# Kernel tuning notes

Hardware: AMD Instinct MI355X
Metric: run time of the kernel (lower is better)

Reference implementation:

```python
import jax, jax.numpy as jnp
import numpy as np
from jax import lax

N, IC, OC, K, SDIM, H, W = 16, 512, 512, 3, 512, 32, 32
PAD, STRIDE, LR = 1, 1, 1.0
WEIGHT_SCALER = 1.0 / np.sqrt(IC * K * K) * LR   # equalized-lr conv scale
FC_SCALER = 1.0 / np.sqrt(SDIM) * LR             # equalized-lr fc scale


def setup_inputs() -> dict:
    key = jax.random.key(0)
    k1, k2, k3 = jax.random.split(key, 3)
    x = jax.random.normal(k1, (N, IC, H, W), dtype=jnp.float32)
    style = jax.random.normal(k2, (N, SDIM), dtype=jnp.float32)
    weight = jax.random.normal(k3, (OC, IC, K, K), dtype=jnp.float32)  # std = 1/lr = 1
    fc_weight = jax.random.normal(jax.random.fold_in(key, 10), (IC, SDIM), dtype=jnp.float32)
    fc_bias = jnp.zeros((IC,), dtype=jnp.float32)
    return {"x": x, "style": style, "weight": weight,
            "fc_weight": fc_weight, "fc_bias": fc_bias}


def reference(x, style, weight, fc_weight, fc_bias):
    # EqualizedFullyConnect + AddChannelwiseBias, then +1 -> modulation rates [N, iC]
    mod = jnp.einsum('ns,cs->nc', style, fc_weight) * FC_SCALER + fc_bias * LR + 1.0
    # modulated per-sample weight [N, oC, iC, kH, kW]
    w = WEIGHT_SCALER * weight[None] * mod[:, None, :, None, None]
    # demodulate: rsqrt of sum of squares over (iC, kH, kW)
    demod = lax.rsqrt(jnp.sum(w * w, axis=(2, 3, 4)) + 1e-8)  # [N, oC]
    w = w * demod[:, :, None, None, None]
    # grouped conv with groups=N == per-sample conv: vmap over batch
    def conv1(xi, wi):
        # xi: [iC,H,W], wi: [oC,iC,kH,kW]
        return lax.conv_general_dilated(
            xi[None], wi, window_strides=(STRIDE, STRIDE),
            padding=((PAD, PAD), (PAD, PAD)),
            dimension_numbers=('NCHW', 'OIHW', 'NCHW'))[0]
    out = jax.vmap(conv1)(x, w)  # [N, oC, H, W]
    return out
```

## Files before the change

kernel.cpp:

```cpp
#include <hip/hip_runtime.h>
#include <hip/hip_bf16.h>

#define N_    16
#define IC_   512
#define OC_   512
#define SDIM_ 512
#define H_    32
#define W_    32
#define HW_   1024

#define FC_SCALER 0.04419417382415922f
#define WS_       0.014731391274719738f
#define WS2_      (1.0f/4608.0f)

typedef __attribute__((__ext_vector_type__(8)))  __bf16 bf16x8;
typedef __attribute__((__ext_vector_type__(16))) float  f32x16;
typedef __attribute__((__ext_vector_type__(4)))  int    i32x4;

typedef __attribute__((address_space(1))) const unsigned int GInt;
typedef __attribute__((address_space(3))) unsigned int LInt;

#define WAIT3()  asm volatile("s_waitcnt vmcnt(3)"  ::: "memory")
#define WAIT8()  asm volatile("s_waitcnt vmcnt(8)"  ::: "memory")
#define WAIT0()  asm volatile("s_waitcnt vmcnt(0)"  ::: "memory")

__device__ __forceinline__ unsigned short f2bf(float f) {
    unsigned int u = __builtin_bit_cast(unsigned int, f);
    unsigned int r = (u + 0x7FFFu + ((u >> 16) & 1u)) >> 16;
    return (unsigned short)r;
}

__global__ void k_mod(const float* __restrict__ style, const float* __restrict__ fcw,
                      const float* __restrict__ fcb, float* __restrict__ mod) {
    int gid = blockIdx.x * blockDim.x + threadIdx.x;
    int wid = gid >> 6, lane = gid & 63;
    if (wid >= N_ * IC_) return;
    int n = wid >> 9, c = wid & 511;
    const float4* sp = (const float4*)(style + n * SDIM_);
    const float4* wp = (const float4*)(fcw + (size_t)c * SDIM_);
    float acc = 0.f;
    for (int i = lane; i < SDIM_ / 4; i += 64) {
        float4 a = sp[i], b = wp[i];
        acc += a.x*b.x + a.y*b.y + a.z*b.z + a.w*b.w;
    }
#pragma unroll
    for (int off = 32; off; off >>= 1) acc += __shfl_xor(acc, off);
    if (lane == 0) mod[wid] = acc * FC_SCALER + fcb[c] + 1.0f;
}

__global__ void k_wprep(const float* __restrict__ w, unsigned short* __restrict__ wt,
                        float* __restrict__ wsq) {
    int tid = blockIdx.x * blockDim.x + threadIdx.x;
    int oc = tid >> 9, ic = tid & 511;
    int og = oc >> 6, ocl = oc & 63;
    int icc = ic >> 5, ks = (ic >> 3) & 3, i8 = ic & 7;
    float s = 0.f;
#pragma unroll
    for (int t = 0; t < 9; t++) {
        float v = w[(size_t)tid * 9 + t];
        s += v * v;
        size_t off = (((size_t)t * 8 + og) * 16 + icc) * 2048
                   + (size_t)ks * 512 + ocl * 8 + i8;
        wt[off] = f2bf(v);
    }
    wsq[tid] = s;
}

__global__ void k_demod(const float* __restrict__ mod, const float* __restrict__ wsq,
                        float* __restrict__ demod_ws) {
    int gid = blockIdx.x * blockDim.x + threadIdx.x;
    int wid = gid >> 6, lane = gid & 63;
    if (wid >= N_ * OC_) return;
    int n = wid >> 9, oc = wid & 511;
    const float4* mp = (const float4*)(mod + n * IC_);
    const float4* qp = (const float4*)(wsq + (size_t)oc * IC_);
    float acc = 0.f;
    for (int i = lane; i < IC_ / 4; i += 64) {
        float4 m = mp[i], q = qp[i];
        acc += m.x*m.x*q.x + m.y*m.y*q.y + m.z*m.z*q.z + m.w*m.w*q.w;
    }
#pragma unroll
    for (int off = 32; off; off >>= 1) acc += __shfl_xor(acc, off);
    if (lane == 0) {
        float s = WS2_ * acc + 1e-8f;
        demod_ws[wid] = WS_ / sqrtf(s);
    }
}

__global__ void k_premod(const float* __restrict__ x, const float* __restrict__ mod,
                         unsigned short* __restrict__ xm) {
    __shared__ __align__(16) unsigned short t_lds[64][80];
    int bx = blockIdx.x;
    int n = bx >> 7, hwt = (bx >> 3) & 15, ict = bx & 7;
    int hw0 = hwt * 64, ic0 = ict * 64;
    int tid = threadIdx.x, lane = tid & 63, ty = tid >> 6;
#pragma unroll
    for (int jj = 0; jj < 16; jj++) {
        int icl = ty * 16 + jj;
        float v = x[(size_t)(n * IC_ + ic0 + icl) * HW_ + hw0 + lane]
                  * mod[n * IC_ + ic0 + icl];
        t_lds[lane][icl] = f2bf(v);
    }
    __syncthreads();
    int xcol = tid & 31, ks64 = tid >> 5;
    int icc = ict * 2 + (ks64 >> 2), ks = ks64 & 3;
#pragma unroll
    for (int rep = 0; rep < 2; rep++) {
        int hwl = rep * 32 + xcol;
        i32x4 v = *(const i32x4*)&t_lds[hwl][ks64 * 8];
        int y = (hw0 >> 5) + rep;
        size_t off = ((((size_t)n * 16 + icc) * 32 + y) * 4 + ks) * 256 + xcol * 8;
        *(i32x4*)(xm + off) = v;
    }
}

__global__ __launch_bounds__(256, 2)
void k_conv(const unsigned short* __restrict__ xm, const unsigned short* __restrict__ wt,
            const float* __restrict__ demod_ws, float* __restrict__ out) {
    __shared__ __align__(16) char smem[79136];
    unsigned short* xt0     = (unsigned short*)(smem);
    unsigned short* wb0     = (unsigned short*)(smem + 40960);
    unsigned short* trash   = (unsigned short*)(smem + 77824);
    float*          zslot   = (float*)(smem + 78848);
    float*          s_demod = (float*)(smem + 78880);

    int bx = blockIdx.x;
    int x8 = bx & 7, j = bx >> 3;
    int n = x8 * 2 + (j >> 5);
    int rem = j & 31;
    int octg = rem >> 2, spt = rem & 3;
    int oc0 = octg * 64, y0 = spt * 8;

    int tid = threadIdx.x, lane = tid & 63, wid = tid >> 6;
    int l31 = lane & 31, lhi = lane >> 5;
    int wc = wid & 1, kh = wid >> 1;

    if (tid < 64) s_demod[tid] = demod_ws[n * OC_ + oc0 + tid];
    __builtin_amdgcn_sched_barrier(0);

    if (tid == 0) { i32x4 z = {}; *(i32x4*)zslot = z; }
    if (spt == 0 && tid < 128) {
        i32x4 z = {};
        *(i32x4*)&xt0[tid * 8] = z;
        *(i32x4*)&xt0[10240 + tid * 8] = z;
    }
    if (spt == 3 && tid < 128) {
        i32x4 z = {};
        *(i32x4*)&xt0[9 * 1024 + tid * 8] = z;
        *(i32x4*)&xt0[10240 + 9 * 1024 + tid * 8] = z;
    }

    const unsigned short* xsrc_n = xm + (size_t)n * (16 * 32 * 1024);

    auto stage_x = [&](int buf, int icc) {
#pragma unroll
        for (int k = 0; k < 5; k++) {
            int c = wid + k * 4;
            int rr = c >> 1, hh = c & 1;
            int y = y0 - 1 + rr;
            bool oob = ((unsigned)y >= 32u) | (icc >= 16);
            int yc = y < 0 ? 0 : (y > 31 ? 31 : y);
            int iccc = icc & 15;
            const unsigned short* g =
                xsrc_n + ((size_t)iccc * 32 + yc) * 1024 + hh * 512 + lane * 8;
            unsigned short* l = oob ? trash
                                    : xt0 + buf * 10240 + rr * 1024 + hh * 512;
            __builtin_amdgcn_global_load_lds((GInt*)g, (LInt*)l, 16, 0, 0);
        }
    };
    auto stage_w = [&](int g2) {
        int gc = g2 < 48 ? g2 : 47;
        int icc2 = gc / 3, p2 = gc % 3;
        bool oob = g2 >= 48;
#pragma unroll
        for (int k = 0; k < 3; k++) {
            int tap = k * 3 + p2;
            const unsigned short* g =
                wt + (((size_t)tap * 8 + octg) * 16 + icc2) * 2048 + wid * 512 + lane * 8;
            unsigned short* l = oob ? trash
                                    : wb0 + (g2 % 3) * 6144 + k * 2048 + wid * 512;
            __builtin_amdgcn_global_load_lds((GInt*)g, (LInt*)l, 16, 0, 0);
        }
    };

    f32x16 acc[2][4] = {};

    stage_x(0, 0);
    stage_w(0);
    stage_w(1);
    asm volatile("s_waitcnt lgkmcnt(0)" ::: "memory");

    int xb = 0;
    int kso = kh * 2 + lhi;
#pragma unroll 1
    for (int icc = 0; icc < 16; icc++) {
#pragma unroll 1
        for (int p = 0; p < 3; p++) {
            int g = icc * 3 + p;
            if (p == 0) WAIT3(); else WAIT8();
            __builtin_amdgcn_s_barrier();
            stage_w(g + 2);
            if (p == 0) stage_x(xb ^ 1, icc + 1);

            const unsigned short* xtb = xt0 + xb * 10240;
            const unsigned short* wbp = wb0 + (g % 3) * 6144;
            int col = l31 + p - 1;
            bool oobc = (unsigned)col >= 32u;
            bf16x8 r6[6];
#pragma unroll
            for (int jj = 0; jj < 6; jj++) {
                int rr = wc * 4 + jj;
                const unsigned short* src = oobc ? (const unsigned short*)zslot
                    : xtb + rr * 1024 + kso * 256 + col * 8;
                r6[jj] = *(const bf16x8*)src;
            }
#pragma unroll
            for (int dy = 0; dy < 3; dy++) {
                bf16x8 af0 = *(const bf16x8*)(wbp + dy * 2048 + kso * 512 + l31 * 8);
                bf16x8 af1 = *(const bf16x8*)(wbp + dy * 2048 + kso * 512 + (32 + l31) * 8);
                __builtin_amdgcn_s_setprio(1);
#pragma unroll
                for (int fs = 0; fs < 4; fs++)
                    acc[0][fs] = __builtin_amdgcn_mfma_f32_32x32x16_bf16(
                        af0, r6[fs + dy], acc[0][fs], 0, 0, 0);
#pragma unroll
                for (int fs = 0; fs < 4; fs++)
                    acc[1][fs] = __builtin_amdgcn_mfma_f32_32x32x16_bf16(
                        af1, r6[fs + dy], acc[1][fs], 0, 0, 0);
                __builtin_amdgcn_s_setprio(0);
            }
        }
        xb ^= 1;
    }

    WAIT0();
    __syncthreads();
    float* exch = (float*)smem;
    if (kh == 1) {
#pragma unroll
        for (int fo = 0; fo < 2; fo++)
#pragma unroll
            for (int fs = 0; fs < 4; fs++)
#pragma unroll
                for (int rg = 0; rg < 16; rg++)
                    exch[(((wc * 2 + fo) * 4 + fs) * 16 + rg) * 64 + lane] = acc[fo][fs][rg];
    }
    __syncthreads();
    if (kh == 0) {
#pragma unroll
        for (int fo = 0; fo < 2; fo++) {
#pragma unroll
            for (int fs = 0; fs < 4; fs++) {
                int y = y0 + wc * 4 + fs;
#pragma unroll
                for (int rg = 0; rg < 16; rg++) {
                    int row = (rg & 3) + 8 * (rg >> 2) + 4 * lhi;
                    int ocl = fo * 32 + row;
                    float v = acc[fo][fs][rg]
                            + exch[(((wc * 2 + fo) * 4 + fs) * 16 + rg) * 64 + lane];
                    v *= s_demod[ocl];
                    out[((size_t)(n * OC_ + oc0 + ocl) * H_ + y) * W_ + l31] = v;
                }
            }
        }
    }
}

extern "C" void kernel_launch(void* const* d_in, const int* in_sizes, int n_in,
                              void* d_out, int out_size, void* d_ws, size_t ws_size,
                              hipStream_t stream) {
    const float* x      = (const float*)d_in[0];
    const float* style  = (const float*)d_in[1];
    const float* weight = (const float*)d_in[2];
    const float* fcw    = (const float*)d_in[3];
    const float* fcb    = (const float*)d_in[4];
    float* out = (float*)d_out;

    char* ws = (char*)d_ws;
    float*          mod   = (float*)ws;
    float*          demod = (float*)(ws + 32768);
    float*          wsq   = (float*)(ws + 65536);
    unsigned short* wtb   = (unsigned short*)(ws + 65536 + 1048576);
    unsigned short* xmb   = (unsigned short*)(ws + 65536 + 1048576 + 4718592);

    k_mod   <<<2048, 256, 0, stream>>>(style, fcw, fcb, mod);
    k_wprep <<<1024, 256, 0, stream>>>(weight, wtb, wsq);
    k_demod <<<2048, 256, 0, stream>>>(mod, wsq, demod);
    k_premod<<<2048, 256, 0, stream>>>(x, mod, xmb);
    k_conv  <<<512,  256, 0, stream>>>(xmb, wtb, demod, out);
}
```

Before: 99.99 us.

## Fuse input modulation and bf16 conversion into conv kernel via register staging

Removes the separate premodulation kernel and its bf16 intermediate buffer. The conv kernel now loads fp32 x rows into registers two channel chunks ahead, multiplies by per-channel modulation held in LDS, packs to bf16 and writes into the LDS x tile. The pipeline is restructured with explicit vmcnt waits and barriers to overlap these loads with the MFMA work. This saves one launch and a global round trip for the intermediate, but the conv kernel now reads twice as many input bytes and uses 40 extra staging registers, which may lower occupancy or stall the pipeline.

Result: no change. 99.71 us (-0.3%).

```diff
diff --git a/kernel.cpp b/kernel.cpp
--- a/kernel.cpp
+++ b/kernel.cpp
@@ -21,8 +21,11 @@
 typedef __attribute__((address_space(3))) unsigned int LInt;
 
 #define WAIT3()  asm volatile("s_waitcnt vmcnt(3)"  ::: "memory")
-#define WAIT8()  asm volatile("s_waitcnt vmcnt(8)"  ::: "memory")
+#define WAIT43() asm volatile("s_waitcnt vmcnt(43)" ::: "memory")
+#define WAIT46() asm volatile("s_waitcnt vmcnt(46)" ::: "memory")
 #define WAIT0()  asm volatile("s_waitcnt vmcnt(0)"  ::: "memory")
+#define LGKM0()  asm volatile("s_waitcnt lgkmcnt(0)" ::: "memory")
+#define SB()     __builtin_amdgcn_sched_barrier(0)
 
 __device__ __forceinline__ unsigned short f2bf(float f) {
     unsigned int u = __builtin_bit_cast(unsigned int, f);
@@ -87,47 +90,22 @@
     }
 }
 
-__global__ void k_premod(const float* __restrict__ x, const float* __restrict__ mod,
-                         unsigned short* __restrict__ xm) {
-    __shared__ __align__(16) unsigned short t_lds[64][80];
-    int bx = blockIdx.x;
-    int n = bx >> 7, hwt = (bx >> 3) & 15, ict = bx & 7;
-    int hw0 = hwt * 64, ic0 = ict * 64;
-    int tid = threadIdx.x, lane = tid & 63, ty = tid >> 6;
-#pragma unroll
-    for (int jj = 0; jj < 16; jj++) {
-        int icl = ty * 16 + jj;
-        float v = x[(size_t)(n * IC_ + ic0 + icl) * HW_ + hw0 + lane]
-                  * mod[n * IC_ + ic0 + icl];
-        t_lds[lane][icl] = f2bf(v);
-    }
-    __syncthreads();
-    int xcol = tid & 31, ks64 = tid >> 5;
-    int icc = ict * 2 + (ks64 >> 2), ks = ks64 & 3;
-#pragma unroll
-    for (int rep = 0; rep < 2; rep++) {
-        int hwl = rep * 32 + xcol;
-        i32x4 v = *(const i32x4*)&t_lds[hwl][ks64 * 8];
-        int y = (hw0 >> 5) + rep;
-        size_t off = ((((size_t)n * 16 + icc) * 32 + y) * 4 + ks) * 256 + xcol * 8;
-        *(i32x4*)(xm + off) = v;
-    }
-}
-
 __global__ __launch_bounds__(256, 2)
-void k_conv(const unsigned short* __restrict__ xm, const unsigned short* __restrict__ wt,
+void k_conv(const float* __restrict__ x, const float* __restrict__ mod,
+            const unsigned short* __restrict__ wt,
             const float* __restrict__ demod_ws, float* __restrict__ out) {
-    __shared__ __align__(16) char smem[79136];
+    __shared__ __align__(16) char smem[81184];
     unsigned short* xt0     = (unsigned short*)(smem);
     unsigned short* wb0     = (unsigned short*)(smem + 40960);
     unsigned short* trash   = (unsigned short*)(smem + 77824);
     float*          zslot   = (float*)(smem + 78848);
     float*          s_demod = (float*)(smem + 78880);
+    float*          mod_lds = (float*)(smem + 79136);
 
     int bx = blockIdx.x;
-    int x8 = bx & 7, j = bx >> 3;
-    int n = x8 * 2 + (j >> 5);
-    int rem = j & 31;
+    int x8 = bx & 7, jj = bx >> 3;
+    int n = x8 * 2 + (jj >> 5);
+    int rem = jj & 31;
     int octg = rem >> 2, spt = rem & 3;
     int oc0 = octg * 64, y0 = spt * 8;
 
@@ -136,36 +114,46 @@
     int wc = wid & 1, kh = wid >> 1;
 
     if (tid < 64) s_demod[tid] = demod_ws[n * OC_ + oc0 + tid];
-    __builtin_amdgcn_sched_barrier(0);
-
+    if (tid < 128) ((float4*)mod_lds)[tid] = ((const float4*)(mod + n * IC_))[tid];
     if (tid == 0) { i32x4 z = {}; *(i32x4*)zslot = z; }
-    if (spt == 0 && tid < 128) {
-        i32x4 z = {};
-        *(i32x4*)&xt0[tid * 8] = z;
-        *(i32x4*)&xt0[10240 + tid * 8] = z;
-    }
-    if (spt == 3 && tid < 128) {
-        i32x4 z = {};
-        *(i32x4*)&xt0[9 * 1024 + tid * 8] = z;
-        *(i32x4*)&xt0[10240 + 9 * 1024 + tid * 8] = z;
-    }
-
-    const unsigned short* xsrc_n = xm + (size_t)n * (16 * 32 * 1024);
-
-    auto stage_x = [&](int buf, int icc) {
+    SB();
+
+    const float* xsrc = x + (size_t)n * IC_ * HW_;
+
+    float xr[5][8];
+    auto stage_xregs = [&](int icc) {
 #pragma unroll
         for (int k = 0; k < 5; k++) {
-            int c = wid + k * 4;
-            int rr = c >> 1, hh = c & 1;
+            int rr = lhi + 2 * k;
             int y = y0 - 1 + rr;
-            bool oob = ((unsigned)y >= 32u) | (icc >= 16);
             int yc = y < 0 ? 0 : (y > 31 ? 31 : y);
-            int iccc = icc & 15;
-            const unsigned short* g =
-                xsrc_n + ((size_t)iccc * 32 + yc) * 1024 + hh * 512 + lane * 8;
-            unsigned short* l = oob ? trash
-                                    : xt0 + buf * 10240 + rr * 1024 + hh * 512;
-            __builtin_amdgcn_global_load_lds((GInt*)g, (LInt*)l, 16, 0, 0);
+            const float* base = xsrc + ((size_t)(icc * 32 + wid * 8)) * HW_ + yc * 32 + l31;
+#pragma unroll
+            for (int i = 0; i < 8; i++) xr[k][i] = base[(size_t)i * HW_];
+        }
+    };
+    auto cvt_store = [&](int icct, int buf) {
+        int mi = (icct & 15) * 32 + wid * 8;
+        float4 mA = *(const float4*)&mod_lds[mi];
+        float4 mB = *(const float4*)&mod_lds[mi + 4];
+#pragma unroll
+        for (int k = 0; k < 5; k++) {
+            int rr = lhi + 2 * k;
+            int y = y0 - 1 + rr;
+            bool oob = (unsigned)y >= 32u;
+            unsigned r0 = 0, r1 = 0, r2 = 0, r3 = 0;
+            if (!oob) {
+                float f0 = xr[k][0]*mA.x, f1 = xr[k][1]*mA.y;
+                float f2 = xr[k][2]*mA.z, f3 = xr[k][3]*mA.w;
+                float f4 = xr[k][4]*mB.x, f5 = xr[k][5]*mB.y;
+                float f6 = xr[k][6]*mB.z, f7 = xr[k][7]*mB.w;
+                asm("v_cvt_pk_bf16_f32 %0, %1, %2" : "=v"(r0) : "v"(f0), "v"(f1));
+                asm("v_cvt_pk_bf16_f32 %0, %1, %2" : "=v"(r1) : "v"(f2), "v"(f3));
+                asm("v_cvt_pk_bf16_f32 %0, %1, %2" : "=v"(r2) : "v"(f4), "v"(f5));
+                asm("v_cvt_pk_bf16_f32 %0, %1, %2" : "=v"(r3) : "v"(f6), "v"(f7));
+            }
+            i32x4 v = { (int)r0, (int)r1, (int)r2, (int)r3 };
+            *(i32x4*)(xt0 + buf * 10240 + rr * 1024 + wid * 256 + l31 * 8) = v;
         }
     };
     auto stage_w = [&](int g2) {
@@ -184,52 +172,100 @@
     };
 
     f32x16 acc[2][4] = {};
-
-    stage_x(0, 0);
-    stage_w(0);
-    stage_w(1);
-    asm volatile("s_waitcnt lgkmcnt(0)" ::: "memory");
-
     int xb = 0;
     int kso = kh * 2 + lhi;
+
+    auto compute = [&](int p, const unsigned short* wbp) {
+        const unsigned short* xtb = xt0 + xb * 10240;
+        int col = l31 + p - 1;
+        bool oobc = (unsigned)col >= 32u;
+        bf16x8 r6[6];
+#pragma unroll
+        for (int j = 0; j < 6; j++) {
+            int rr = wc * 4 + j;
+            const unsigned short* src = oobc ? (const unsigned short*)zslot
+                : xtb + rr * 1024 + kso * 256 + col * 8;
+            r6[j] = *(const bf16x8*)src;
+        }
+#pragma unroll
+        for (int dy = 0; dy < 3; dy++) {
+            bf16x8 af0 = *(const bf16x8*)(wbp + dy * 2048 + kso * 512 + l31 * 8);
+            bf16x8 af1 = *(const bf16x8*)(wbp + dy * 2048 + kso * 512 + (32 + l31) * 8);
+            __builtin_amdgcn_s_setprio(1);
+#pragma unroll
+            for (int fs = 0; fs < 4; fs++)
+                acc[0][fs] = __builtin_amdgcn_mfma_f32_32x32x16_bf16(
+                    af0, r6[fs + dy], acc[0][fs], 0, 0, 0);
+#pragma unroll
+            for (int fs = 0; fs < 4; fs++)
+                acc[1][fs] = __builtin_amdgcn_mfma_f32_32x32x16_bf16(
+                    af1, r6[fs + dy], acc[1][fs], 0, 0, 0);
+            __builtin_amdgcn_s_setprio(0);
+        }
+    };
+
+    stage_xregs(0); SB();
+    float x0r[5][8];
+#pragma unroll
+    for (int k = 0; k < 5; k++)
+#pragma unroll
+        for (int i = 0; i < 8; i++) x0r[k][i] = xr[k][i];
+    stage_xregs(1); SB();
+    stage_w(0); stage_w(1); SB();
+    WAIT46();
+    LGKM0();
+    __builtin_amdgcn_s_barrier();
+    {
+        int mi = 0 * 32 + wid * 8;
+        float4 mA = *(const float4*)&mod_lds[mi];
+        float4 mB = *(const float4*)&mod_lds[mi + 4];
+#pragma unroll
+        for (int k = 0; k < 5; k++) {
+            int rr = lhi + 2 * k;
+            int y = y0 - 1 + rr;
+            bool oob = (unsigned)y >= 32u;
+            unsigned r0 = 0, r1 = 0, r2 = 0, r3 = 0;
+            if (!oob) {
+                float f0 = x0r[k][0]*mA.x, f1 = x0r[k][1]*mA.y;
+                float f2 = x0r[k][2]*mA.z, f3 = x0r[k][3]*mA.w;
+                float f4 = x0r[k][4]*mB.x, f5 = x0r[k][5]*mB.y;
+                float f6 = x0r[k][6]*mB.z, f7 = x0r[k][7]*mB.w;
+                asm("v_cvt_pk_bf16_f32 %0, %1, %2" : "=v"(r0) : "v"(f0), "v"(f1));
+                asm("v_cvt_pk_bf16_f32 %0, %1, %2" : "=v"(r1) : "v"(f2), "v"(f3));
+                asm("v_cvt_pk_bf16_f32 %0, %1, %2" : "=v"(r2) : "v"(f4), "v"(f5));
+                asm("v_cvt_pk_bf16_f32 %0, %1, %2" : "=v"(r3) : "v"(f6), "v"(f7));
+            }
+            i32x4 v = { (int)r0, (int)r1, (int)r2, (int)r3 };
+            *(i32x4*)(xt0 + rr * 1024 + wid * 256 + l31 * 8) = v;
+        }
+    }
+    SB();
+
 #pragma unroll 1
     for (int icc = 0; icc < 16; icc++) {
-#pragma unroll 1
-        for (int p = 0; p < 3; p++) {
-            int g = icc * 3 + p;
-            if (p == 0) WAIT3(); else WAIT8();
-            __builtin_amdgcn_s_barrier();
-            stage_w(g + 2);
-            if (p == 0) stage_x(xb ^ 1, icc + 1);
-
-            const unsigned short* xtb = xt0 + xb * 10240;
-            const unsigned short* wbp = wb0 + (g % 3) * 6144;
-            int col = l31 + p - 1;
-            bool oobc = (unsigned)col >= 32u;
-            bf16x8 r6[6];
-#pragma unroll
-            for (int jj = 0; jj < 6; jj++) {
-                int rr = wc * 4 + jj;
-                const unsigned short* src = oobc ? (const unsigned short*)zslot
-                    : xtb + rr * 1024 + kso * 256 + col * 8;
-                r6[jj] = *(const bf16x8*)src;
-            }
-#pragma unroll
-            for (int dy = 0; dy < 3; dy++) {
-                bf16x8 af0 = *(const bf16x8*)(wbp + dy * 2048 + kso * 512 + l31 * 8);
-                bf16x8 af1 = *(const bf16x8*)(wbp + dy * 2048 + kso * 512 + (32 + l31) * 8);
-                __builtin_amdgcn_s_setprio(1);
-#pragma unroll
-                for (int fs = 0; fs < 4; fs++)
-                    acc[0][fs] = __builtin_amdgcn_mfma_f32_32x32x16_bf16(
-                        af0, r6[fs + dy], acc[0][fs], 0, 0, 0);
-#pragma unroll
-                for (int fs = 0; fs < 4; fs++)
-                    acc[1][fs] = __builtin_amdgcn_mfma_f32_32x32x16_bf16(
-                        af1, r6[fs + dy], acc[1][fs], 0, 0, 0);
-                __builtin_amdgcn_s_setprio(0);
-            }
-        }
+        int g0 = icc * 3;
+        WAIT3();
+        LGKM0();
+        __builtin_amdgcn_s_barrier();
+        cvt_store(icc + 1, xb ^ 1);
+        SB();
+        stage_w(g0 + 2);
+        SB();
+        stage_xregs((icc + 2) & 15);
+        SB();
+        compute(0, wb0 + (g0 % 3) * 6144);
+        WAIT43();
+        LGKM0();
+        __builtin_amdgcn_s_barrier();
+        stage_w(g0 + 3);
+        SB();
+        compute(1, wb0 + ((g0 + 1) % 3) * 6144);
+        WAIT43();
+        LGKM0();
+        __builtin_amdgcn_s_barrier();
+        stage_w(g0 + 4);
+        SB();
+        compute(2, wb0 + ((g0 + 2) % 3) * 6144);
         xb ^= 1;
     }
 
@@ -281,11 +317,9 @@
     float*          demod = (float*)(ws + 32768);
     float*          wsq   = (float*)(ws + 65536);
     unsigned short* wtb   = (unsigned short*)(ws + 65536 + 1048576);
-    unsigned short* xmb   = (unsigned short*)(ws + 65536 + 1048576 + 4718592);
 
     k_mod   <<<2048, 256, 0, stream>>>(style, fcw, fcb, mod);
     k_wprep <<<1024, 256, 0, stream>>>(weight, wtb, wsq);
     k_demod <<<2048, 256, 0, stream>>>(mod, wsq, demod);
-    k_premod<<<2048, 256, 0, stream>>>(x, mod, xmb);
-    k_conv  <<<512,  256, 0, stream>>>(xmb, wtb, demod, out);
-}
+    k_conv  <<<512,  256, 0, stream>>>(x, mod, wtb, demod, out);
+}
```

## Load conv weight fragments directly into registers instead of staging through LDS

Applied to the files above, without the earlier changes.

Weight A-fragments are now fetched straight from global memory into a triple-buffered register set, with the phase loop unrolled into explicit compute/fetch stages. The LDS weight ring buffer is removed. The epilogue exchange is split per output-half so that LDS drops from about 79KB to 42KB, which may allow more blocks per CU. The block-to-(n, oc-group) mapping across XCDs is also reshuffled for better L2 locality of weights. The costs are higher VGPR pressure from 18 extra bf16x8 registers and per-wave redundant global weight loads that are no longer shared through LDS.

Result: no change. 101.8 us (+1.8%).

```diff
diff --git a/kernel.cpp b/kernel.cpp
--- a/kernel.cpp
+++ b/kernel.cpp
@@ -20,9 +20,10 @@
 typedef __attribute__((address_space(1))) const unsigned int GInt;
 typedef __attribute__((address_space(3))) unsigned int LInt;
 
-#define WAIT3()  asm volatile("s_waitcnt vmcnt(3)"  ::: "memory")
-#define WAIT8()  asm volatile("s_waitcnt vmcnt(8)"  ::: "memory")
+#define WAIT12() asm volatile("s_waitcnt vmcnt(12)" ::: "memory")
 #define WAIT0()  asm volatile("s_waitcnt vmcnt(0)"  ::: "memory")
+#define LGKM0()  asm volatile("s_waitcnt lgkmcnt(0)" ::: "memory")
+#define SB()     __builtin_amdgcn_sched_barrier(0)
 
 __device__ __forceinline__ unsigned short f2bf(float f) {
     unsigned int u = __builtin_bit_cast(unsigned int, f);
@@ -117,27 +118,25 @@
 __global__ __launch_bounds__(256, 2)
 void k_conv(const unsigned short* __restrict__ xm, const unsigned short* __restrict__ wt,
             const float* __restrict__ demod_ws, float* __restrict__ out) {
-    __shared__ __align__(16) char smem[79136];
+    __shared__ __align__(16) char smem[42304];
     unsigned short* xt0     = (unsigned short*)(smem);
-    unsigned short* wb0     = (unsigned short*)(smem + 40960);
-    unsigned short* trash   = (unsigned short*)(smem + 77824);
-    float*          zslot   = (float*)(smem + 78848);
-    float*          s_demod = (float*)(smem + 78880);
+    unsigned short* trash   = (unsigned short*)(smem + 40960);
+    float*          zslot   = (float*)(smem + 41984);
+    float*          s_demod = (float*)(smem + 42016);
 
     int bx = blockIdx.x;
-    int x8 = bx & 7, j = bx >> 3;
-    int n = x8 * 2 + (j >> 5);
-    int rem = j & 31;
-    int octg = rem >> 2, spt = rem & 3;
+    int xcd = bx & 7, j = bx >> 3;
+    int h = xcd & 1, q = xcd >> 1;
+    int a = j >> 4, b = (j >> 2) & 3, s = j & 3;
+    int octg = h * 4 + a, n = q * 4 + b, spt = s;
     int oc0 = octg * 64, y0 = spt * 8;
 
     int tid = threadIdx.x, lane = tid & 63, wid = tid >> 6;
     int l31 = lane & 31, lhi = lane >> 5;
     int wc = wid & 1, kh = wid >> 1;
+    int kso = kh * 2 + lhi;
 
     if (tid < 64) s_demod[tid] = demod_ws[n * OC_ + oc0 + tid];
-    __builtin_amdgcn_sched_barrier(0);
-
     if (tid == 0) { i32x4 z = {}; *(i32x4*)zslot = z; }
     if (spt == 0 && tid < 128) {
         i32x4 z = {};
@@ -149,6 +148,8 @@
         *(i32x4*)&xt0[9 * 1024 + tid * 8] = z;
         *(i32x4*)&xt0[10240 + 9 * 1024 + tid * 8] = z;
     }
+    WAIT0();
+    SB();
 
     const unsigned short* xsrc_n = xm + (size_t)n * (16 * 32 * 1024);
 
@@ -168,87 +169,92 @@
             __builtin_amdgcn_global_load_lds((GInt*)g, (LInt*)l, 16, 0, 0);
         }
     };
-    auto stage_w = [&](int g2) {
+    auto fetch_A = [&](int g2, bf16x8 (&dst)[6]) {
         int gc = g2 < 48 ? g2 : 47;
-        int icc2 = gc / 3, p2 = gc % 3;
-        bool oob = g2 >= 48;
-#pragma unroll
-        for (int k = 0; k < 3; k++) {
-            int tap = k * 3 + p2;
-            const unsigned short* g =
-                wt + (((size_t)tap * 8 + octg) * 16 + icc2) * 2048 + wid * 512 + lane * 8;
-            unsigned short* l = oob ? trash
-                                    : wb0 + (g2 % 3) * 6144 + k * 2048 + wid * 512;
-            __builtin_amdgcn_global_load_lds((GInt*)g, (LInt*)l, 16, 0, 0);
+        int icc2 = gc / 3, p2 = gc - icc2 * 3;
+#pragma unroll
+        for (int dy = 0; dy < 3; dy++) {
+            int tap = dy * 3 + p2;
+            const unsigned short* base =
+                wt + (((size_t)tap * 8 + octg) * 16 + icc2) * 2048 + kso * 512 + l31 * 8;
+            dst[dy * 2 + 0] = *(const bf16x8*)(base);
+            dst[dy * 2 + 1] = *(const bf16x8*)(base + 256);
         }
     };
 
     f32x16 acc[2][4] = {};
+    int xb = 0;
+
+    auto compute = [&](int p, const bf16x8 (&wAv)[6]) {
+        const unsigned short* xtb = xt0 + xb * 10240;
+        int col = l31 + p - 1;
+        bool oobc = (unsigned)col >= 32u;
+        bf16x8 r6[6];
+#pragma unroll
+        for (int jj2 = 0; jj2 < 6; jj2++) {
+            int rr = wc * 4 + jj2;
+            const unsigned short* src = oobc ? (const unsigned short*)zslot
+                : xtb + rr * 1024 + kso * 256 + col * 8;
+            r6[jj2] = *(const bf16x8*)src;
+        }
+#pragma unroll
+        for (int dy = 0; dy < 3; dy++) {
+            __builtin_amdgcn_s_setprio(1);
+#pragma unroll
+            for (int fs = 0; fs < 4; fs++)
+                acc[0][fs] = __builtin_amdgcn_mfma_f32_32x32x16_bf16(
+                    wAv[dy * 2 + 0], r6[fs + dy], acc[0][fs], 0, 0, 0);
+#pragma unroll
+            for (int fs = 0; fs < 4; fs++)
+                acc[1][fs] = __builtin_amdgcn_mfma_f32_32x32x16_bf16(
+                    wAv[dy * 2 + 1], r6[fs + dy], acc[1][fs], 0, 0, 0);
+            __builtin_amdgcn_s_setprio(0);
+        }
+    };
+
+    bf16x8 wS0[6], wS1[6], wS2[6];
 
     stage_x(0, 0);
-    stage_w(0);
-    stage_w(1);
-    asm volatile("s_waitcnt lgkmcnt(0)" ::: "memory");
-
-    int xb = 0;
-    int kso = kh * 2 + lhi;
+    fetch_A(0, wS0);
+    fetch_A(1, wS1);
+    LGKM0();
+
 #pragma unroll 1
     for (int icc = 0; icc < 16; icc++) {
-#pragma unroll 1
-        for (int p = 0; p < 3; p++) {
-            int g = icc * 3 + p;
-            if (p == 0) WAIT3(); else WAIT8();
-            __builtin_amdgcn_s_barrier();
-            stage_w(g + 2);
-            if (p == 0) stage_x(xb ^ 1, icc + 1);
-
-            const unsigned short* xtb = xt0 + xb * 10240;
-            const unsigned short* wbp = wb0 + (g % 3) * 6144;
-            int col = l31 + p - 1;
-            bool oobc = (unsigned)col >= 32u;
-            bf16x8 r6[6];
-#pragma unroll
-            for (int jj = 0; jj < 6; jj++) {
-                int rr = wc * 4 + jj;
-                const unsigned short* src = oobc ? (const unsigned short*)zslot
-                    : xtb + rr * 1024 + kso * 256 + col * 8;
-                r6[jj] = *(const bf16x8*)src;
-            }
-#pragma unroll
-            for (int dy = 0; dy < 3; dy++) {
-                bf16x8 af0 = *(const bf16x8*)(wbp + dy * 2048 + kso * 512 + l31 * 8);
-                bf16x8 af1 = *(const bf16x8*)(wbp + dy * 2048 + kso * 512 + (32 + l31) * 8);
-                __builtin_amdgcn_s_setprio(1);
-#pragma unroll
-                for (int fs = 0; fs < 4; fs++)
-                    acc[0][fs] = __builtin_amdgcn_mfma_f32_32x32x16_bf16(
-                        af0, r6[fs + dy], acc[0][fs], 0, 0, 0);
-#pragma unroll
-                for (int fs = 0; fs < 4; fs++)
-                    acc[1][fs] = __builtin_amdgcn_mfma_f32_32x32x16_bf16(
-                        af1, r6[fs + dy], acc[1][fs], 0, 0, 0);
-                __builtin_amdgcn_s_setprio(0);
-            }
-        }
+        int g0 = icc * 3;
+        WAIT12();
+        __builtin_amdgcn_s_barrier();
+        SB();
+        fetch_A(g0 + 2, wS2);
+        stage_x(xb ^ 1, icc + 1);
+        SB();
+        compute(0, wS0);
+        SB();
+        fetch_A(g0 + 3, wS0);
+        SB();
+        compute(1, wS1);
+        SB();
+        fetch_A(g0 + 4, wS1);
+        SB();
+        compute(2, wS2);
+        SB();
         xb ^= 1;
     }
 
     WAIT0();
     __syncthreads();
     float* exch = (float*)smem;
-    if (kh == 1) {
-#pragma unroll
-        for (int fo = 0; fo < 2; fo++)
+#pragma unroll
+    for (int fo = 0; fo < 2; fo++) {
+        if (kh == 1) {
 #pragma unroll
             for (int fs = 0; fs < 4; fs++)
 #pragma unroll
                 for (int rg = 0; rg < 16; rg++)
-                    exch[(((wc * 2 + fo) * 4 + fs) * 16 + rg) * 64 + lane] = acc[fo][fs][rg];
-    }
-    __syncthreads();
-    if (kh == 0) {
-#pragma unroll
-        for (int fo = 0; fo < 2; fo++) {
+                    exch[((wc * 4 + fs) * 16 + rg) * 64 + lane] = acc[fo][fs][rg];
+        }
+        __syncthreads();
+        if (kh == 0) {
 #pragma unroll
             for (int fs = 0; fs < 4; fs++) {
                 int y = y0 + wc * 4 + fs;
@@ -257,12 +263,13 @@
                     int row = (rg & 3) + 8 * (rg >> 2) + 4 * lhi;
                     int ocl = fo * 32 + row;
                     float v = acc[fo][fs][rg]
-                            + exch[(((wc * 2 + fo) * 4 + fs) * 16 + rg) * 64 + lane];
+                            + exch[((wc * 4 + fs) * 16 + rg) * 64 + lane];
                     v *= s_demod[ocl];
                     out[((size_t)(n * OC_ + oc0 + ocl) * H_ + y) * W_ + l31] = v;
                 }
             }
         }
+        __syncthreads();
     }
 }
 
```
